# Performance work log

Measured on AMD Instinct MI355X. Metric: run time of the kernel, lower is better.

The kernel has to match this reference:

```python
import jax, jax.numpy as jnp
import numpy as np

T, H, I, E, K = 2048, 1024, 768, 32, 4  # tokens, hidden, expert intermediate, n_experts, top_k


def setup_inputs() -> dict:
    key = jax.random.key(0)
    k0, k1, k2, k3, k4 = jax.random.split(key, 5)
    scale = 0.02
    return {
        "x": jax.random.normal(k0, (T, H), dtype=jnp.float32),
        "gate_w": jax.random.normal(k1, (E, H), dtype=jnp.float32) * scale,   # router linear [E, H]
        "w_gate": jax.random.normal(k2, (E, I, H), dtype=jnp.float32) * scale,  # gate_proj per expert
        "w_up": jax.random.normal(k3, (E, I, H), dtype=jnp.float32) * scale,    # up_proj per expert
        "w_down": jax.random.normal(k4, (E, H, I), dtype=jnp.float32) * scale,  # down_proj per expert
    }


def reference(x, gate_w, w_gate, w_up, w_down):
    # Router: dense gate linear + softmax + top-k + renormalize
    logits = x @ gate_w.T                              # [T, E]
    probs = jax.nn.softmax(logits, axis=-1)
    top_w, top_i = jax.lax.top_k(probs, K)             # [T, K]
    top_w = top_w / jnp.sum(top_w, axis=-1, keepdims=True)  # renormalize=True
    # Dense combine weights [T, E] (zero for unselected experts)
    tok = jnp.arange(T, dtype=jnp.int32)[:, None]
    combine = jnp.zeros((T, E), dtype=x.dtype).at[tok, top_i].add(top_w)

    # Scan over experts: each expert is a SwiGLU MLP; masked-dense combine.
    def step(acc, ws):
        w1, w3, w2, ce = ws                            # [I,H], [I,H], [H,I], [T]
        h = (jax.nn.silu(x @ w1.T) * (x @ w3.T)) @ w2.T  # [T, H]
        return acc + ce[:, None] * h, None

    out, _ = jax.lax.scan(step, jnp.zeros_like(x), (w_gate, w_up, w_down, combine.T))
    return out
```

## Files before the change

kernel.cpp:

```cpp
#include <hip/hip_runtime.h>
#include <hip/hip_bf16.h>
#include <stdint.h>

#define T_TOK 2048
#define HDIM  1024
#define IDIM  768
#define NEXP  32
#define TOPK  4
#define NPAIR (T_TOK*TOPK)

typedef __attribute__((ext_vector_type(8))) short bf16x8;
typedef __attribute__((ext_vector_type(4))) float f32x4;

typedef __attribute__((address_space(1))) const unsigned int gu32;
typedef __attribute__((address_space(3))) unsigned int lu32;

__device__ __forceinline__ void gload_lds16(const void* g, void* l){
  __builtin_amdgcn_global_load_lds((gu32*)g, (lu32*)l, 16, 0, 0);
}

__device__ __forceinline__ unsigned short f2bf(float f){
  union { float f; unsigned u; } v; v.f = f;
  unsigned r = (v.u + 0x7fffu + ((v.u >> 16) & 1u)) >> 16;
  return (unsigned short)r;
}

__global__ __launch_bounds__(256) void k_convert_x(const float* __restrict__ x,
                                                   ushort* __restrict__ xb){
  int idx = blockIdx.x*256 + threadIdx.x;
  float4 v = ((const float4*)x)[idx];
  ushort4 o; o.x=f2bf(v.x); o.y=f2bf(v.y); o.z=f2bf(v.z); o.w=f2bf(v.w);
  ((ushort4*)xb)[idx] = o;
}

__global__ __launch_bounds__(256) void k_router(const float* __restrict__ x,
                                                const float* __restrict__ gw,
                                                int* __restrict__ ei, float* __restrict__ wv,
                                                int* __restrict__ counts){
  int wid  = threadIdx.x >> 6;
  int lane = threadIdx.x & 63;
  int t = blockIdx.x*4 + wid;
  float xv[16];
  #pragma unroll
  for (int i=0;i<16;i++) xv[i] = x[t*HDIM + i*64 + lane];
  float p[NEXP];
  #pragma unroll
  for (int e=0;e<NEXP;e++){
    const float* w = gw + e*HDIM;
    float a = 0.f;
    #pragma unroll
    for (int i=0;i<16;i++) a = fmaf(xv[i], w[i*64+lane], a);
    #pragma unroll
    for (int off=32; off>=1; off>>=1) a += __shfl_xor(a, off, 64);
    p[e] = a;
  }
  float m = p[0];
  #pragma unroll
  for (int e=1;e<NEXP;e++) m = fmaxf(m, p[e]);
  #pragma unroll
  for (int e=0;e<NEXP;e++) p[e] = __expf(p[e]-m);
  unsigned used = 0; int sel[TOPK]; float sw[TOPK]; float wsum = 0.f;
  #pragma unroll
  for (int k=0;k<TOPK;k++){
    float best = -1.f; int bi = 0;
    #pragma unroll
    for (int e=0;e<NEXP;e++){
      bool ok = (((used>>e)&1u)==0u) && (p[e] > best);
      best = ok ? p[e] : best; bi = ok ? e : bi;
    }
    used |= 1u<<bi; sel[k]=bi; sw[k]=best; wsum += best;
  }
  if (lane==0){
    float inv = 1.f/wsum;
    #pragma unroll
    for (int k=0;k<TOPK;k++){
      ei[t*TOPK+k] = sel[k];
      wv[t*TOPK+k] = sw[k]*inv;
      atomicAdd(&counts[sel[k]], 1);
    }
  }
}

__global__ void k_offsets(const int* __restrict__ counts, int* __restrict__ offsets){
  if (threadIdx.x==0 && blockIdx.x==0){
    int s=0;
    for (int e=0;e<NEXP;e++){ offsets[e]=s; s+=counts[e]; }
    offsets[NEXP]=s;
  }
}

__global__ __launch_bounds__(256) void k_scatter(const int* __restrict__ ei,
                                                 const int* __restrict__ offsets,
                                                 int* __restrict__ cursor,
                                                 int* __restrict__ slot_tk,
                                                 int* __restrict__ tk_slot){
  int g = blockIdx.x*256 + threadIdx.x;
  int e = ei[g];
  int pos = atomicAdd(&cursor[e], 1);
  int slot = offsets[e] + pos;
  slot_tk[slot] = g;
  tk_slot[g] = slot;
}

__global__ __launch_bounds__(512) void k_gateup(const ushort* __restrict__ xb,
    const float* __restrict__ w1, const float* __restrict__ w3,
    const int* __restrict__ offsets, const int* __restrict__ slot_tk,
    ushort* __restrict__ act){
  int flat = blockIdx.x;
  int e    = (flat & 7) + 8*((flat>>3)&3);
  int it   = (flat>>5)&7;
  int mt   = flat>>8;
  int off0 = offsets[e];
  int ne   = offsets[e+1]-off0;
  int m0   = mt*256;
  if (m0 >= ne) return;
  int ibase = it*96;

  __shared__ int toks[256];
  __shared__ ushort Als[2][256][64];
  __shared__ ushort Bls[2][2][96][72];

  int tid = threadIdx.x, wid = tid>>6, lane = tid&63;
  if (tid < 256){
    int slot = off0 + m0 + tid;
    int fb = slot_tk[off0] >> 2;
    toks[tid] = (m0 + tid < ne) ? (slot_tk[slot] >> 2) : fb;
  }
  __syncthreads();

  const ushort* asrc[4];
  int schunk = (lane&7) ^ (lane>>3);
  #pragma unroll
  for (int s=0;s<4;s++){
    int row = wid*32 + s*8 + (lane>>3);
    asrc[s] = xb + (size_t)toks[row]*HDIM + schunk*8;
  }
  const float* bsrc[6]; int b_mat[6], b_r[6], b_c4[6];
  const size_t wbase = (size_t)e * IDIM * HDIM;
  #pragma unroll
  for (int s=0;s<6;s++){
    int li = s*512 + tid;
    int mat = (li >= 1536) ? 1 : 0;
    int li2 = li - mat*1536;
    int r = li2>>4, c4 = li2&15;
    b_mat[s]=mat; b_r[s]=r; b_c4[s]=c4;
    bsrc[s] = (mat ? w3 : w1) + wbase + (size_t)(ibase+r)*HDIM + c4*4;
  }

  int wm = wid >> 1, wn = wid & 1;
  f32x4 accg[4][3], accu[4][3];
  #pragma unroll
  for (int a=0;a<4;a++)
    #pragma unroll
    for (int b=0;b<3;b++){ accg[a][b]=(f32x4){0,0,0,0}; accu[a][b]=(f32x4){0,0,0,0}; }

  float4 breg[6];
  #pragma unroll
  for (int s=0;s<6;s++) breg[s] = *(const float4*)(bsrc[s]);
  #pragma unroll
  for (int s=0;s<4;s++) gload_lds16(asrc[s], &Als[0][wid*32+s*8][0]);
  #pragma unroll
  for (int s=0;s<6;s++){
    ushort4 o; o.x=f2bf(breg[s].x); o.y=f2bf(breg[s].y); o.z=f2bf(breg[s].z); o.w=f2bf(breg[s].w);
    *(ushort4*)(&Bls[0][b_mat[s]][b_r[s]][b_c4[s]*4]) = o;
  }
  __syncthreads();

  for (int kb=0; kb<16; ++kb){
    int cur = kb & 1, nxt = cur ^ 1;
    if (kb < 15){
      #pragma unroll
      for (int s=0;s<6;s++) breg[s] = *(const float4*)(bsrc[s] + (kb+1)*64);
      #pragma unroll
      for (int s=0;s<4;s++) gload_lds16(asrc[s] + (kb+1)*64, &Als[nxt][wid*32+s*8][0]);
    }
    #pragma unroll
    for (int kk=0; kk<2; ++kk){
      bf16x8 af[4];
      #pragma unroll
      for (int m=0;m<4;m++){
        int row = wm*64 + m*16 + (lane&15);
        int ch  = (kk*4 + (lane>>4)) ^ (lane&7);
        af[m] = *(const bf16x8*)(&Als[cur][row][ch*8]);
      }
      #pragma unroll
      for (int n=0;n<3;n++){
        bf16x8 bg = *(const bf16x8*)(&Bls[cur][0][wn*48 + n*16 + (lane&15)][kk*32 + (lane>>4)*8]);
        bf16x8 bu = *(const bf16x8*)(&Bls[cur][1][wn*48 + n*16 + (lane&15)][kk*32 + (lane>>4)*8]);
        #pragma unroll
        for (int m=0;m<4;m++){
          accg[m][n] = __builtin_amdgcn_mfma_f32_16x16x32_bf16(af[m], bg, accg[m][n], 0,0,0);
          accu[m][n] = __builtin_amdgcn_mfma_f32_16x16x32_bf16(af[m], bu, accu[m][n], 0,0,0);
        }
      }
    }
    if (kb < 15){
      #pragma unroll
      for (int s=0;s<6;s++){
        ushort4 o; o.x=f2bf(breg[s].x); o.y=f2bf(breg[s].y); o.z=f2bf(breg[s].z); o.w=f2bf(breg[s].w);
        *(ushort4*)(&Bls[nxt][b_mat[s]][b_r[s]][b_c4[s]*4]) = o;
      }
    }
    __syncthreads();
  }

  int nval = ne - m0; if (nval > 256) nval = 256;
  #pragma unroll
  for (int m=0;m<4;m++)
    #pragma unroll
    for (int n=0;n<3;n++)
      #pragma unroll
      for (int r=0;r<4;r++){
        int row = wm*64 + m*16 + (lane>>4)*4 + r;
        if (row < nval){
          float g = accg[m][n][r], u = accu[m][n][r];
          float sval = g / (1.f + __expf(-g)) * u;
          act[(size_t)(off0+m0+row)*IDIM + ibase + wn*48 + n*16 + (lane&15)] = f2bf(sval);
        }
      }
}

__global__ __launch_bounds__(512) void k_down(const ushort* __restrict__ act,
    const float* __restrict__ w2, const int* __restrict__ offsets,
    float* __restrict__ pout){
  int flat = blockIdx.x;
  int e    = (flat & 7) + 8*((flat>>3)&3);
  int ht   = (flat>>5)&7;
  int mt   = flat>>8;
  int off0 = offsets[e], ne = offsets[e+1]-off0;
  int m0   = mt*256;
  if (m0 >= ne) return;
  int hbase = ht*128;

  __shared__ ushort Als[2][256][64];
  __shared__ ushort Bls[2][128][72];

  int tid = threadIdx.x, wid = tid>>6, lane = tid&63;
  int wm = wid>>1, wn = wid&1;

  const ushort* asrc[4];
  int schunk = (lane&7) ^ (lane>>3);
  #pragma unroll
  for (int s=0;s<4;s++){
    int row = wid*32 + s*8 + (lane>>3);
    int mrow = m0 + row; mrow = (mrow < ne) ? mrow : (ne-1);
    asrc[s] = act + (size_t)(off0+mrow)*IDIM + schunk*8;
  }
  const float* bsrc[4]; int b_r[4], b_c4[4];
  const size_t wbase = (size_t)e * HDIM * IDIM;
  #pragma unroll
  for (int s=0;s<4;s++){
    int li = s*512 + tid;
    int r = li>>4, c4 = li&15;
    b_r[s]=r; b_c4[s]=c4;
    bsrc[s] = w2 + wbase + (size_t)(hbase+r)*IDIM + c4*4;
  }

  f32x4 acc[4][4];
  #pragma unroll
  for (int a=0;a<4;a++)
    #pragma unroll
    for (int b=0;b<4;b++) acc[a][b]=(f32x4){0,0,0,0};

  float4 breg[4];
  #pragma unroll
  for (int s=0;s<4;s++) breg[s] = *(const float4*)(bsrc[s]);
  #pragma unroll
  for (int s=0;s<4;s++) gload_lds16(asrc[s], &Als[0][wid*32+s*8][0]);
  #pragma unroll
  for (int s=0;s<4;s++){
    ushort4 o; o.x=f2bf(breg[s].x); o.y=f2bf(breg[s].y); o.z=f2bf(breg[s].z); o.w=f2bf(breg[s].w);
    *(ushort4*)(&Bls[0][b_r[s]][b_c4[s]*4]) = o;
  }
  __syncthreads();

  for (int kb=0; kb<12; ++kb){
    int cur = kb & 1, nxt = cur ^ 1;
    if (kb < 11){
      #pragma unroll
      for (int s=0;s<4;s++) breg[s] = *(const float4*)(bsrc[s] + (kb+1)*64);
      #pragma unroll
      for (int s=0;s<4;s++) gload_lds16(asrc[s] + (kb+1)*64, &Als[nxt][wid*32+s*8][0]);
    }
    #pragma unroll
    for (int kk=0; kk<2; ++kk){
      bf16x8 af[4];
      #pragma unroll
      for (int m=0;m<4;m++){
        int row = wm*64 + m*16 + (lane&15);
        int ch  = (kk*4 + (lane>>4)) ^ (lane&7);
        af[m] = *(const bf16x8*)(&Als[cur][row][ch*8]);
      }
      #pragma unroll
      for (int n=0;n<4;n++){
        bf16x8 bw = *(const bf16x8*)(&Bls[cur][wn*64 + n*16 + (lane&15)][kk*32 + (lane>>4)*8]);
        #pragma unroll
        for (int m=0;m<4;m++)
          acc[m][n] = __builtin_amdgcn_mfma_f32_16x16x32_bf16(af[m], bw, acc[m][n], 0,0,0);
      }
    }
    if (kb < 11){
      #pragma unroll
      for (int s=0;s<4;s++){
        ushort4 o; o.x=f2bf(breg[s].x); o.y=f2bf(breg[s].y); o.z=f2bf(breg[s].z); o.w=f2bf(breg[s].w);
        *(ushort4*)(&Bls[nxt][b_r[s]][b_c4[s]*4]) = o;
      }
    }
    __syncthreads();
  }

  int nval = ne - m0; if (nval > 256) nval = 256;
  #pragma unroll
  for (int m=0;m<4;m++)
    #pragma unroll
    for (int n=0;n<4;n++)
      #pragma unroll
      for (int r=0;r<4;r++){
        int row = wm*64 + m*16 + (lane>>4)*4 + r;
        if (row < nval)
          pout[(size_t)(off0+m0+row)*HDIM + hbase + wn*64 + n*16 + (lane&15)] = acc[m][n][r];
      }
}

__global__ __launch_bounds__(256) void k_combine(const float* __restrict__ pout,
    const int* __restrict__ tk_slot, const float* __restrict__ wv,
    float* __restrict__ out){
  int t = blockIdx.x;
  int c = threadIdx.x;
  float a0=0,a1=0,a2=0,a3=0;
  #pragma unroll
  for (int k=0;k<TOPK;k++){
    int slot = tk_slot[t*TOPK+k];
    float w  = wv[t*TOPK+k];
    float4 v = *(const float4*)(pout + (size_t)slot*HDIM + c*4);
    a0 = fmaf(w, v.x, a0); a1 = fmaf(w, v.y, a1);
    a2 = fmaf(w, v.z, a2); a3 = fmaf(w, v.w, a3);
  }
  float4 o; o.x=a0; o.y=a1; o.z=a2; o.w=a3;
  *(float4*)(out + (size_t)t*HDIM + c*4) = o;
}

extern "C" void kernel_launch(void* const* d_in, const int* in_sizes, int n_in,
                              void* d_out, int out_size, void* d_ws, size_t ws_size,
                              hipStream_t stream){
  const float* x  = (const float*)d_in[0];
  const float* gw = (const float*)d_in[1];
  const float* w1 = (const float*)d_in[2];
  const float* w3 = (const float*)d_in[3];
  const float* w2 = (const float*)d_in[4];
  float* out = (float*)d_out;

  char* ws = (char*)d_ws;
  size_t off = 0;
  ushort* xb   = (ushort*)(ws + off); off += (size_t)T_TOK*HDIM*2;
  ushort* act  = (ushort*)(ws + off); off += (size_t)NPAIR*IDIM*2;
  float*  pout = (float*) (ws + off); off += (size_t)NPAIR*HDIM*4;
  int* counts  = (int*)(ws + off); off += NEXP*4;
  int* cursor  = (int*)(ws + off); off += NEXP*4;
  int* offsets = (int*)(ws + off); off += (NEXP+1)*4;
  off = (off + 255) & ~(size_t)255;
  int*   ei      = (int*)  (ws + off); off += (size_t)NPAIR*4;
  float* wvp     = (float*)(ws + off); off += (size_t)NPAIR*4;
  int*   slot_tk = (int*)  (ws + off); off += (size_t)NPAIR*4;
  int*   tk_slot = (int*)  (ws + off); off += (size_t)NPAIR*4;

  hipMemsetAsync(counts, 0, 2*NEXP*4, stream);

  k_convert_x<<<T_TOK*HDIM/1024, 256, 0, stream>>>(x, xb);
  k_router<<<T_TOK/4, 256, 0, stream>>>(x, gw, ei, wvp, counts);
  k_offsets<<<1, 64, 0, stream>>>(counts, offsets);
  k_scatter<<<NPAIR/256, 256, 0, stream>>>(ei, offsets, cursor, slot_tk, tk_slot);
  k_gateup<<<512, 512, 0, stream>>>(xb, w1, w3, offsets, slot_tk, act);
  k_down<<<512, 512, 0, stream>>>(act, w2, offsets, pout);
  k_combine<<<T_TOK, 256, 0, stream>>>(pout, tk_slot, wvp, out);
}
```

Before: 253.2 us.

## Compact expert M-tile list and read activations directly from global memory

Builds a compacted list of (expert, m0) tiles in k_offsets so the gate/up and down GEMMs launch only over real work, with no fixed 8-tile-per-expert grid. The N tile shrinks (48 intermediate, 64 hidden columns per block) and the A-operand LDS staging is removed in favour of direct per-lane global loads of the activations. The smaller LDS and register footprint plus launch bounds of 4 are meant to raise occupancy and spread work over more blocks. In exchange, A fragments are reloaded from global or L2 with no LDS reuse, and B weights are re-converted by more blocks. MAXMT=64 silently caps the tile count, which only holds when tokens are spread evenly across experts.

```diff
diff --git a/kernel.cpp b/kernel.cpp
--- a/kernel.cpp
+++ b/kernel.cpp
@@ -8,16 +8,11 @@
 #define NEXP  32
 #define TOPK  4
 #define NPAIR (T_TOK*TOPK)
+#define MTILE 256
+#define MAXMT 64
 
 typedef __attribute__((ext_vector_type(8))) short bf16x8;
 typedef __attribute__((ext_vector_type(4))) float f32x4;
-
-typedef __attribute__((address_space(1))) const unsigned int gu32;
-typedef __attribute__((address_space(3))) unsigned int lu32;
-
-__device__ __forceinline__ void gload_lds16(const void* g, void* l){
-  __builtin_amdgcn_global_load_lds((gu32*)g, (lu32*)l, 16, 0, 0);
-}
 
 __device__ __forceinline__ unsigned short f2bf(float f){
   union { float f; unsigned u; } v; v.f = f;
@@ -81,11 +76,19 @@
   }
 }
 
-__global__ void k_offsets(const int* __restrict__ counts, int* __restrict__ offsets){
+__global__ void k_offsets(const int* __restrict__ counts, int* __restrict__ offsets,
+                          int* __restrict__ mtE, int* __restrict__ mtM0,
+                          int* __restrict__ nmt){
   if (threadIdx.x==0 && blockIdx.x==0){
     int s=0;
     for (int e=0;e<NEXP;e++){ offsets[e]=s; s+=counts[e]; }
     offsets[NEXP]=s;
+    int nm=0;
+    for (int e=0;e<NEXP;e++){
+      int ne = counts[e];
+      for (int m0=0; m0<ne && nm<MAXMT; m0+=MTILE){ mtE[nm]=e; mtM0[nm]=m0; nm++; }
+    }
+    nmt[0]=nm;
   }
 }
 
@@ -102,23 +105,23 @@
   tk_slot[g] = slot;
 }
 
-__global__ __launch_bounds__(512) void k_gateup(const ushort* __restrict__ xb,
+__global__ __launch_bounds__(512,4) void k_gateup(const ushort* __restrict__ xb,
     const float* __restrict__ w1, const float* __restrict__ w3,
     const int* __restrict__ offsets, const int* __restrict__ slot_tk,
+    const int* __restrict__ mtE, const int* __restrict__ mtM0, const int* __restrict__ nmt,
     ushort* __restrict__ act){
-  int flat = blockIdx.x;
-  int e    = (flat & 7) + 8*((flat>>3)&3);
-  int it   = (flat>>5)&7;
-  int mt   = flat>>8;
+  int bi  = blockIdx.x;
+  int mti = bi >> 4;
+  int it  = bi & 15;
+  if (mti >= nmt[0]) return;
+  int e    = mtE[mti];
+  int m0   = mtM0[mti];
   int off0 = offsets[e];
   int ne   = offsets[e+1]-off0;
-  int m0   = mt*256;
-  if (m0 >= ne) return;
-  int ibase = it*96;
+  int ibase = it*48;
 
   __shared__ int toks[256];
-  __shared__ ushort Als[2][256][64];
-  __shared__ ushort Bls[2][2][96][72];
+  __shared__ ushort Bls[2][2][48][68];
 
   int tid = threadIdx.x, wid = tid>>6, lane = tid&63;
   if (tid < 256){
@@ -126,41 +129,37 @@
     int fb = slot_tk[off0] >> 2;
     toks[tid] = (m0 + tid < ne) ? (slot_tk[slot] >> 2) : fb;
   }
-  __syncthreads();
-
-  const ushort* asrc[4];
-  int schunk = (lane&7) ^ (lane>>3);
-  #pragma unroll
-  for (int s=0;s<4;s++){
-    int row = wid*32 + s*8 + (lane>>3);
-    asrc[s] = xb + (size_t)toks[row]*HDIM + schunk*8;
-  }
-  const float* bsrc[6]; int b_mat[6], b_r[6], b_c4[6];
+  const float* bsrc[3]; int b_mat[3], b_r[3], b_c4[3];
   const size_t wbase = (size_t)e * IDIM * HDIM;
   #pragma unroll
-  for (int s=0;s<6;s++){
+  for (int s=0;s<3;s++){
     int li = s*512 + tid;
-    int mat = (li >= 1536) ? 1 : 0;
-    int li2 = li - mat*1536;
+    int mat = li >= 768;
+    int li2 = li - mat*768;
     int r = li2>>4, c4 = li2&15;
     b_mat[s]=mat; b_r[s]=r; b_c4[s]=c4;
     bsrc[s] = (mat ? w3 : w1) + wbase + (size_t)(ibase+r)*HDIM + c4*4;
   }
-
-  int wm = wid >> 1, wn = wid & 1;
-  f32x4 accg[4][3], accu[4][3];
-  #pragma unroll
-  for (int a=0;a<4;a++)
+  __syncthreads();
+
+  const ushort* arow[2];
+  #pragma unroll
+  for (int m=0;m<2;m++){
+    int row = wid*32 + m*16 + (lane&15);
+    arow[m] = xb + (size_t)toks[row]*HDIM + (lane>>4)*8;
+  }
+
+  f32x4 accg[2][3], accu[2][3];
+  #pragma unroll
+  for (int a=0;a<2;a++)
     #pragma unroll
     for (int b=0;b<3;b++){ accg[a][b]=(f32x4){0,0,0,0}; accu[a][b]=(f32x4){0,0,0,0}; }
 
-  float4 breg[6];
-  #pragma unroll
-  for (int s=0;s<6;s++) breg[s] = *(const float4*)(bsrc[s]);
-  #pragma unroll
-  for (int s=0;s<4;s++) gload_lds16(asrc[s], &Als[0][wid*32+s*8][0]);
-  #pragma unroll
-  for (int s=0;s<6;s++){
+  float4 breg[3];
+  #pragma unroll
+  for (int s=0;s<3;s++) breg[s] = *(const float4*)(bsrc[s]);
+  #pragma unroll
+  for (int s=0;s<3;s++){
     ushort4 o; o.x=f2bf(breg[s].x); o.y=f2bf(breg[s].y); o.z=f2bf(breg[s].z); o.w=f2bf(breg[s].w);
     *(ushort4*)(&Bls[0][b_mat[s]][b_r[s]][b_c4[s]*4]) = o;
   }
@@ -170,25 +169,20 @@
     int cur = kb & 1, nxt = cur ^ 1;
     if (kb < 15){
       #pragma unroll
-      for (int s=0;s<6;s++) breg[s] = *(const float4*)(bsrc[s] + (kb+1)*64);
-      #pragma unroll
-      for (int s=0;s<4;s++) gload_lds16(asrc[s] + (kb+1)*64, &Als[nxt][wid*32+s*8][0]);
+      for (int s=0;s<3;s++) breg[s] = *(const float4*)(bsrc[s] + (kb+1)*64);
     }
     #pragma unroll
     for (int kk=0; kk<2; ++kk){
-      bf16x8 af[4];
-      #pragma unroll
-      for (int m=0;m<4;m++){
-        int row = wm*64 + m*16 + (lane&15);
-        int ch  = (kk*4 + (lane>>4)) ^ (lane&7);
-        af[m] = *(const bf16x8*)(&Als[cur][row][ch*8]);
-      }
+      bf16x8 af[2];
+      #pragma unroll
+      for (int m=0;m<2;m++)
+        af[m] = *(const bf16x8*)(arow[m] + kb*64 + kk*32);
       #pragma unroll
       for (int n=0;n<3;n++){
-        bf16x8 bg = *(const bf16x8*)(&Bls[cur][0][wn*48 + n*16 + (lane&15)][kk*32 + (lane>>4)*8]);
-        bf16x8 bu = *(const bf16x8*)(&Bls[cur][1][wn*48 + n*16 + (lane&15)][kk*32 + (lane>>4)*8]);
+        bf16x8 bg = *(const bf16x8*)(&Bls[cur][0][n*16 + (lane&15)][kk*32 + (lane>>4)*8]);
+        bf16x8 bu = *(const bf16x8*)(&Bls[cur][1][n*16 + (lane&15)][kk*32 + (lane>>4)*8]);
         #pragma unroll
-        for (int m=0;m<4;m++){
+        for (int m=0;m<2;m++){
           accg[m][n] = __builtin_amdgcn_mfma_f32_16x16x32_bf16(af[m], bg, accg[m][n], 0,0,0);
           accu[m][n] = __builtin_amdgcn_mfma_f32_16x16x32_bf16(af[m], bu, accu[m][n], 0,0,0);
         }
@@ -196,7 +190,7 @@
     }
     if (kb < 15){
       #pragma unroll
-      for (int s=0;s<6;s++){
+      for (int s=0;s<3;s++){
         ushort4 o; o.x=f2bf(breg[s].x); o.y=f2bf(breg[s].y); o.z=f2bf(breg[s].z); o.w=f2bf(breg[s].w);
         *(ushort4*)(&Bls[nxt][b_mat[s]][b_r[s]][b_c4[s]*4]) = o;
       }
@@ -206,69 +200,66 @@
 
   int nval = ne - m0; if (nval > 256) nval = 256;
   #pragma unroll
-  for (int m=0;m<4;m++)
+  for (int m=0;m<2;m++)
     #pragma unroll
     for (int n=0;n<3;n++)
       #pragma unroll
       for (int r=0;r<4;r++){
-        int row = wm*64 + m*16 + (lane>>4)*4 + r;
+        int row = wid*32 + m*16 + (lane>>4)*4 + r;
         if (row < nval){
           float g = accg[m][n][r], u = accu[m][n][r];
           float sval = g / (1.f + __expf(-g)) * u;
-          act[(size_t)(off0+m0+row)*IDIM + ibase + wn*48 + n*16 + (lane&15)] = f2bf(sval);
+          act[(size_t)(off0+m0+row)*IDIM + ibase + n*16 + (lane&15)] = f2bf(sval);
         }
       }
 }
 
-__global__ __launch_bounds__(512) void k_down(const ushort* __restrict__ act,
+__global__ __launch_bounds__(512,4) void k_down(const ushort* __restrict__ act,
     const float* __restrict__ w2, const int* __restrict__ offsets,
+    const int* __restrict__ mtE, const int* __restrict__ mtM0, const int* __restrict__ nmt,
     float* __restrict__ pout){
-  int flat = blockIdx.x;
-  int e    = (flat & 7) + 8*((flat>>3)&3);
-  int ht   = (flat>>5)&7;
-  int mt   = flat>>8;
+  int bi  = blockIdx.x;
+  int mti = bi >> 4;
+  int ht  = bi & 15;
+  if (mti >= nmt[0]) return;
+  int e    = mtE[mti];
+  int m0   = mtM0[mti];
   int off0 = offsets[e], ne = offsets[e+1]-off0;
-  int m0   = mt*256;
-  if (m0 >= ne) return;
-  int hbase = ht*128;
-
-  __shared__ ushort Als[2][256][64];
-  __shared__ ushort Bls[2][128][72];
+  int hbase = ht*64;
+
+  __shared__ ushort Bls[2][64][68];
 
   int tid = threadIdx.x, wid = tid>>6, lane = tid&63;
-  int wm = wid>>1, wn = wid&1;
-
-  const ushort* asrc[4];
-  int schunk = (lane&7) ^ (lane>>3);
-  #pragma unroll
-  for (int s=0;s<4;s++){
-    int row = wid*32 + s*8 + (lane>>3);
-    int mrow = m0 + row; mrow = (mrow < ne) ? mrow : (ne-1);
-    asrc[s] = act + (size_t)(off0+mrow)*IDIM + schunk*8;
-  }
-  const float* bsrc[4]; int b_r[4], b_c4[4];
+
+  const float* bsrc[2]; int b_r[2], b_c4[2];
   const size_t wbase = (size_t)e * HDIM * IDIM;
   #pragma unroll
-  for (int s=0;s<4;s++){
+  for (int s=0;s<2;s++){
     int li = s*512 + tid;
     int r = li>>4, c4 = li&15;
     b_r[s]=r; b_c4[s]=c4;
     bsrc[s] = w2 + wbase + (size_t)(hbase+r)*IDIM + c4*4;
   }
 
-  f32x4 acc[4][4];
-  #pragma unroll
-  for (int a=0;a<4;a++)
+  const ushort* arow[2];
+  #pragma unroll
+  for (int m=0;m<2;m++){
+    int row = wid*32 + m*16 + (lane&15);
+    int mrow = m0 + row; mrow = (mrow < ne) ? mrow : 0;
+    arow[m] = act + (size_t)(off0+mrow)*IDIM + (lane>>4)*8;
+  }
+
+  f32x4 acc[2][4];
+  #pragma unroll
+  for (int a=0;a<2;a++)
     #pragma unroll
     for (int b=0;b<4;b++) acc[a][b]=(f32x4){0,0,0,0};
 
-  float4 breg[4];
-  #pragma unroll
-  for (int s=0;s<4;s++) breg[s] = *(const float4*)(bsrc[s]);
-  #pragma unroll
-  for (int s=0;s<4;s++) gload_lds16(asrc[s], &Als[0][wid*32+s*8][0]);
-  #pragma unroll
-  for (int s=0;s<4;s++){
+  float4 breg[2];
+  #pragma unroll
+  for (int s=0;s<2;s++) breg[s] = *(const float4*)(bsrc[s]);
+  #pragma unroll
+  for (int s=0;s<2;s++){
     ushort4 o; o.x=f2bf(breg[s].x); o.y=f2bf(breg[s].y); o.z=f2bf(breg[s].z); o.w=f2bf(breg[s].w);
     *(ushort4*)(&Bls[0][b_r[s]][b_c4[s]*4]) = o;
   }
@@ -278,30 +269,25 @@
     int cur = kb & 1, nxt = cur ^ 1;
     if (kb < 11){
       #pragma unroll
-      for (int s=0;s<4;s++) breg[s] = *(const float4*)(bsrc[s] + (kb+1)*64);
-      #pragma unroll
-      for (int s=0;s<4;s++) gload_lds16(asrc[s] + (kb+1)*64, &Als[nxt][wid*32+s*8][0]);
+      for (int s=0;s<2;s++) breg[s] = *(const float4*)(bsrc[s] + (kb+1)*64);
     }
     #pragma unroll
     for (int kk=0; kk<2; ++kk){
-      bf16x8 af[4];
-      #pragma unroll
-      for (int m=0;m<4;m++){
-        int row = wm*64 + m*16 + (lane&15);
-        int ch  = (kk*4 + (lane>>4)) ^ (lane&7);
-        af[m] = *(const bf16x8*)(&Als[cur][row][ch*8]);
-      }
+      bf16x8 af[2];
+      #pragma unroll
+      for (int m=0;m<2;m++)
+        af[m] = *(const bf16x8*)(arow[m] + kb*64 + kk*32);
       #pragma unroll
       for (int n=0;n<4;n++){
-        bf16x8 bw = *(const bf16x8*)(&Bls[cur][wn*64 + n*16 + (lane&15)][kk*32 + (lane>>4)*8]);
+        bf16x8 bw = *(const bf16x8*)(&Bls[cur][n*16 + (lane&15)][kk*32 + (lane>>4)*8]);
         #pragma unroll
-        for (int m=0;m<4;m++)
+        for (int m=0;m<2;m++)
           acc[m][n] = __builtin_amdgcn_mfma_f32_16x16x32_bf16(af[m], bw, acc[m][n], 0,0,0);
       }
     }
     if (kb < 11){
       #pragma unroll
-      for (int s=0;s<4;s++){
+      for (int s=0;s<2;s++){
         ushort4 o; o.x=f2bf(breg[s].x); o.y=f2bf(breg[s].y); o.z=f2bf(breg[s].z); o.w=f2bf(breg[s].w);
         *(ushort4*)(&Bls[nxt][b_r[s]][b_c4[s]*4]) = o;
       }
@@ -311,14 +297,14 @@
 
   int nval = ne - m0; if (nval > 256) nval = 256;
   #pragma unroll
-  for (int m=0;m<4;m++)
+  for (int m=0;m<2;m++)
     #pragma unroll
     for (int n=0;n<4;n++)
       #pragma unroll
       for (int r=0;r<4;r++){
-        int row = wm*64 + m*16 + (lane>>4)*4 + r;
+        int row = wid*32 + m*16 + (lane>>4)*4 + r;
         if (row < nval)
-          pout[(size_t)(off0+m0+row)*HDIM + hbase + wn*64 + n*16 + (lane&15)] = acc[m][n][r];
+          pout[(size_t)(off0+m0+row)*HDIM + hbase + n*16 + (lane&15)] = acc[m][n][r];
       }
 }
 
@@ -358,6 +344,9 @@
   int* counts  = (int*)(ws + off); off += NEXP*4;
   int* cursor  = (int*)(ws + off); off += NEXP*4;
   int* offsets = (int*)(ws + off); off += (NEXP+1)*4;
+  int* mtE     = (int*)(ws + off); off += MAXMT*4;
+  int* mtM0    = (int*)(ws + off); off += MAXMT*4;
+  int* nmt     = (int*)(ws + off); off += 4;
   off = (off + 255) & ~(size_t)255;
   int*   ei      = (int*)  (ws + off); off += (size_t)NPAIR*4;
   float* wvp     = (float*)(ws + off); off += (size_t)NPAIR*4;
@@ -368,9 +357,9 @@
 
   k_convert_x<<<T_TOK*HDIM/1024, 256, 0, stream>>>(x, xb);
   k_router<<<T_TOK/4, 256, 0, stream>>>(x, gw, ei, wvp, counts);
-  k_offsets<<<1, 64, 0, stream>>>(counts, offsets);
+  k_offsets<<<1, 64, 0, stream>>>(counts, offsets, mtE, mtM0, nmt);
   k_scatter<<<NPAIR/256, 256, 0, stream>>>(ei, offsets, cursor, slot_tk, tk_slot);
-  k_gateup<<<512, 512, 0, stream>>>(xb, w1, w3, offsets, slot_tk, act);
-  k_down<<<512, 512, 0, stream>>>(act, w2, offsets, pout);
+  k_gateup<<<MAXMT*16, 512, 0, stream>>>(xb, w1, w3, offsets, slot_tk, mtE, mtM0, nmt, act);
+  k_down<<<MAXMT*16, 512, 0, stream>>>(act, w2, offsets, mtE, mtM0, nmt, pout);
   k_combine<<<T_TOK, 256, 0, stream>>>(pout, tk_slot, wvp, out);
 }
```

Measured after the change: 277.7 us. 9.7% more time.
